# Kernel optimization log

Measured on AMD Instinct MI355X. Metric: run time of the kernel, lower is better.

## Reference

```python
import jax, jax.numpy as jnp
import numpy as np

B, T, C = 4, 2048, 1024
H = 16
D = C // H  # head_size = 64


def setup_inputs() -> dict:
    key = jax.random.key(0)
    ks = jax.random.split(key, 9)
    s = 1.0 / np.sqrt(C)  # keep activations well-scaled
    return {
        "x": jax.random.normal(ks[0], (B, T, C), dtype=jnp.float32),
        "Wq": jax.random.normal(ks[1], (C, C), dtype=jnp.float32) * s,
        "bq": jnp.zeros((C,), dtype=jnp.float32),
        "Wk": jax.random.normal(ks[2], (C, C), dtype=jnp.float32) * s,
        "bk": jnp.zeros((C,), dtype=jnp.float32),
        "Wv": jax.random.normal(ks[3], (C, C), dtype=jnp.float32) * s,
        "bv": jnp.zeros((C,), dtype=jnp.float32),
        "Wp": jax.random.normal(ks[4], (C, C), dtype=jnp.float32) * s,
        "bp": jnp.zeros((C,), dtype=jnp.float32),
    }


def reference(x, Wq, bq, Wk, bk, Wv, bv, Wp, bp):
    # QKV projections: [B,T,C] -> [B,H,T,D]
    def heads(y):
        return y.reshape(B, T, H, D).transpose(0, 2, 1, 3)

    q = heads(x @ Wq + bq)
    k = heads(x @ Wk + bk)
    v = heads(x @ Wv + bv)

    # scaled dot-product attention scores [B,H,T,T]
    attn = jnp.einsum("bhqd,bhkd->bhqk", q, k) * (D ** -0.5)
    causal = jnp.tril(jnp.ones((T, T), dtype=bool))  # [T,T]
    attn = jnp.where(causal[None, None, :, :], attn, -jnp.inf)
    attn = jax.nn.softmax(attn, axis=-1)
    # dropout = 0.0 -> identity

    y = jnp.einsum("bhqk,bhkd->bhqd", attn, v)  # [B,H,T,D]
    y = y.transpose(0, 2, 1, 3).reshape(B, T, C)
    return y @ Wp + bp
```

## Files before the change

kernel.cpp:

```cpp
#include <hip/hip_runtime.h>
#include <math.h>

static constexpr int Bsz = 4;
static constexpr int Tn  = 2048;
static constexpr int Cn  = 1024;
static constexpr int Hn  = 16;
static constexpr int Dn  = 64;

typedef __attribute__((ext_vector_type(8))) short bf16x8;
typedef __attribute__((ext_vector_type(4))) float f32x4;

#define MFMA16(a, b, c) __builtin_amdgcn_mfma_f32_16x16x32_bf16((a), (b), (c), 0, 0, 0)

static constexpr float kQScale = 0.18033688f;

__device__ __forceinline__ unsigned short f2bf(float f) {
  unsigned u = __float_as_uint(f);
  unsigned r = (u + 0x7fffu + ((u >> 16) & 1u)) >> 16;
  return (unsigned short)r;
}

__device__ __forceinline__ unsigned cvtpk_bf16(float lo, float hi) {
  unsigned r;
  asm("v_cvt_pk_bf16_f32 %0, %1, %2" : "=v"(r) : "v"(lo), "v"(hi));
  return r;
}

__device__ __forceinline__ void load_lds16(const void* g, void* l) {
  __builtin_amdgcn_global_load_lds(
      (const __attribute__((address_space(1))) void*)g,
      (__attribute__((address_space(3))) void*)l, 16, 0, 0);
}

__global__ __launch_bounds__(256) void prep_k(
    const float* __restrict__ x, unsigned short* __restrict__ xb,
    const float* __restrict__ w0, const float* __restrict__ w1,
    const float* __restrict__ w2, const float* __restrict__ w3,
    unsigned short* __restrict__ o0, unsigned short* __restrict__ o1,
    unsigned short* __restrict__ o2, unsigned short* __restrict__ o3) {
  __shared__ unsigned short Ts[64][65];
  const int z = blockIdx.z;
  if (z >= 4) {
    const int bi = (z - 4) * 256 + blockIdx.y * 16 + blockIdx.x;
    const int i = bi * 256 + threadIdx.x;
    const float4 a = ((const float4*)x)[i * 2 + 0];
    const float4 b = ((const float4*)x)[i * 2 + 1];
    uint4 o;
    o.x = cvtpk_bf16(a.x, a.y);
    o.y = cvtpk_bf16(a.z, a.w);
    o.z = cvtpk_bf16(b.x, b.y);
    o.w = cvtpk_bf16(b.z, b.w);
    ((uint4*)xb)[i] = o;
    return;
  }
  const float* W;
  unsigned short* O;
  switch (z) {
    case 0: W = w0; O = o0; break;
    case 1: W = w1; O = o1; break;
    case 2: W = w2; O = o2; break;
    default: W = w3; O = o3; break;
  }
  const int k0 = blockIdx.y * 64, n0 = blockIdx.x * 64;
  const int tid = threadIdx.x;
  const int cr = tid >> 4, cc = (tid & 15) * 4;
#pragma unroll
  for (int p = 0; p < 4; ++p) {
    const int r = p * 16 + cr;
    const float4 v = *(const float4*)&W[(size_t)(k0 + r) * Cn + n0 + cc];
    Ts[r][cc + 0] = f2bf(v.x);
    Ts[r][cc + 1] = f2bf(v.y);
    Ts[r][cc + 2] = f2bf(v.z);
    Ts[r][cc + 3] = f2bf(v.w);
  }
  __syncthreads();
#pragma unroll
  for (int p = 0; p < 4; ++p) {
    const int n = p * 16 + cr;
    ushort4 o;
    o.x = Ts[cc + 0][n];
    o.y = Ts[cc + 1][n];
    o.z = Ts[cc + 2][n];
    o.w = Ts[cc + 3][n];
    *(ushort4*)&O[(size_t)(n0 + n) * Cn + k0 + cc] = o;
  }
}

__device__ __forceinline__ void gemm_core(
    const unsigned short* __restrict__ A, const unsigned short* __restrict__ Bt,
    int row0, int col0, unsigned short* As, unsigned short* Bs,
    f32x4 acc[4][4]) {
  const int tid = threadIdx.x;
  const int lane = tid & 63, w = tid >> 6;
  const int wm = w >> 1, wn = w & 1;
  const int lr = lane & 15, lg = lane >> 4;

  auto stage = [&](int buf, int k0) {
#pragma unroll
    for (int it = 0; it < 4; ++it) {
      const int c = it * 256 + tid;
      const int r = c >> 3;
      const int lc = (c & 7) ^ (r & 7);
      load_lds16(A + (size_t)(row0 + r) * Cn + k0 + lc * 8,
                 &As[buf * 8192 + c * 8]);
    }
#pragma unroll
    for (int it = 0; it < 4; ++it) {
      const int c = it * 256 + tid;
      const int r = c >> 3;
      const int lc = (c & 7) ^ (r & 7);
      load_lds16(Bt + (size_t)(col0 + r) * Cn + k0 + lc * 8,
                 &Bs[buf * 8192 + c * 8]);
    }
  };

  stage(0, 0);
  for (int ki = 0; ki < 16; ++ki) {
    const int cur = ki & 1;
    const bool pf = (ki < 15);
    if (pf) stage(cur ^ 1, (ki + 1) * 64);
    if (pf) asm volatile("s_waitcnt vmcnt(8)" ::: "memory");
    else    asm volatile("s_waitcnt vmcnt(0)" ::: "memory");
    __builtin_amdgcn_s_barrier();
#pragma unroll
    for (int ks = 0; ks < 2; ++ks) {
      bf16x8 af[4], bfr[4];
#pragma unroll
      for (int mi = 0; mi < 4; ++mi)
        af[mi] = *(const bf16x8*)
            &As[cur * 8192 + (wm * 64 + mi * 16 + lr) * 64 +
                (((ks * 4 + lg) ^ (lr & 7)) << 3)];
#pragma unroll
      for (int ni = 0; ni < 4; ++ni)
        bfr[ni] = *(const bf16x8*)
            &Bs[cur * 8192 + (wn * 64 + ni * 16 + lr) * 64 +
                (((ks * 4 + lg) ^ (lr & 7)) << 3)];
#pragma unroll
      for (int mi = 0; mi < 4; ++mi)
#pragma unroll
        for (int ni = 0; ni < 4; ++ni)
          acc[mi][ni] = MFMA16(af[mi], bfr[ni], acc[mi][ni]);
    }
    if (pf) __builtin_amdgcn_s_barrier();
  }
}

__global__ __launch_bounds__(256, 2) void qkv_fused_k(
    const unsigned short* __restrict__ A,
    const unsigned short* __restrict__ Wq, const unsigned short* __restrict__ Wk,
    const unsigned short* __restrict__ Wv,
    const float* __restrict__ bq, const float* __restrict__ bk,
    const float* __restrict__ bv,
    unsigned short* __restrict__ Qo, unsigned short* __restrict__ Ko,
    unsigned short* __restrict__ Vo) {
  __shared__ unsigned short As[2][128 * 32];
  __shared__ unsigned short Bs[2][3][128 * 32];
  const int tid = threadIdx.x, lane = tid & 63, w = tid >> 6;
  const int wm = w >> 1, wn = w & 1;
  const int lr = lane & 15, lg = lane >> 4;
  const int row0 = blockIdx.x * 128, col0 = blockIdx.y * 128;

  auto stage = [&](int buf, int k0) {
    const unsigned short* Ws[3] = {Wq, Wk, Wv};
#pragma unroll
    for (int it = 0; it < 2; ++it) {
      const int c = it * 256 + tid;
      const int r = c >> 2;
      const int lc = (c & 3) ^ ((r >> 1) & 3);
      load_lds16(A + (size_t)(row0 + r) * Cn + k0 + lc * 8, &As[buf][c * 8]);
    }
#pragma unroll
    for (int z = 0; z < 3; ++z)
#pragma unroll
      for (int it = 0; it < 2; ++it) {
        const int c = it * 256 + tid;
        const int r = c >> 2;
        const int lc = (c & 3) ^ ((r >> 1) & 3);
        load_lds16(Ws[z] + (size_t)(col0 + r) * Cn + k0 + lc * 8,
                   &Bs[buf][z][c * 8]);
      }
  };

  const f32x4 fz = {0.f, 0.f, 0.f, 0.f};
  f32x4 acc0[4][4], acc1[4][4], acc2[4][4];
#pragma unroll
  for (int i = 0; i < 4; ++i)
#pragma unroll
    for (int j = 0; j < 4; ++j) { acc0[i][j] = fz; acc1[i][j] = fz; acc2[i][j] = fz; }

  stage(0, 0);
  for (int ki = 0; ki < 32; ++ki) {
    const int cur = ki & 1;
    const bool pf = (ki < 31);
    if (pf) stage(cur ^ 1, (ki + 1) * 32);
    if (pf) asm volatile("s_waitcnt vmcnt(8)" ::: "memory");
    else    asm volatile("s_waitcnt vmcnt(0)" ::: "memory");
    __builtin_amdgcn_s_barrier();

    const int kchunk = (lg ^ ((lr >> 1) & 3)) << 3;
    bf16x8 af[4];
#pragma unroll
    for (int mi = 0; mi < 4; ++mi)
      af[mi] = *(const bf16x8*)
          &As[cur][(wm * 64 + mi * 16 + lr) * 32 + kchunk];

    {
      bf16x8 bfr[4];
#pragma unroll
      for (int ni = 0; ni < 4; ++ni)
        bfr[ni] = *(const bf16x8*)
            &Bs[cur][0][(wn * 64 + ni * 16 + lr) * 32 + kchunk];
      __builtin_amdgcn_s_setprio(1);
#pragma unroll
      for (int mi = 0; mi < 4; ++mi)
#pragma unroll
        for (int ni = 0; ni < 4; ++ni)
          acc0[mi][ni] = MFMA16(af[mi], bfr[ni], acc0[mi][ni]);
      __builtin_amdgcn_s_setprio(0);
    }
    {
      bf16x8 bfr[4];
#pragma unroll
      for (int ni = 0; ni < 4; ++ni)
        bfr[ni] = *(const bf16x8*)
            &Bs[cur][1][(wn * 64 + ni * 16 + lr) * 32 + kchunk];
      __builtin_amdgcn_s_setprio(1);
#pragma unroll
      for (int mi = 0; mi < 4; ++mi)
#pragma unroll
        for (int ni = 0; ni < 4; ++ni)
          acc1[mi][ni] = MFMA16(af[mi], bfr[ni], acc1[mi][ni]);
      __builtin_amdgcn_s_setprio(0);
    }
    {
      bf16x8 bfr[4];
#pragma unroll
      for (int ni = 0; ni < 4; ++ni)
        bfr[ni] = *(const bf16x8*)
            &Bs[cur][2][(wn * 64 + ni * 16 + lr) * 32 + kchunk];
      __builtin_amdgcn_s_setprio(1);
#pragma unroll
      for (int mi = 0; mi < 4; ++mi)
#pragma unroll
        for (int ni = 0; ni < 4; ++ni)
          acc2[mi][ni] = MFMA16(af[mi], bfr[ni], acc2[mi][ni]);
      __builtin_amdgcn_s_setprio(0);
    }

    if (pf) __builtin_amdgcn_s_barrier();
  }

  const int b = row0 >> 11;
  const int t0w = (row0 & (Tn - 1)) + wm * 64;
  const int h = (col0 >> 6) + wn;

#pragma unroll
  for (int mi = 0; mi < 4; ++mi) {
#pragma unroll
    for (int ni = 0; ni < 4; ++ni) {
      const int d = ni * 16 + lr;
      const float bv_ = bv[col0 + wn * 64 + d];
      const int t0 = t0w + mi * 16 + lg * 4;
      ushort4 o4;
      o4.x = f2bf(acc2[mi][ni][0] + bv_);
      o4.y = f2bf(acc2[mi][ni][1] + bv_);
      o4.z = f2bf(acc2[mi][ni][2] + bv_);
      o4.w = f2bf(acc2[mi][ni][3] + bv_);
      *(ushort4*)&Vo[(((size_t)b * Hn + h) * Dn + d) * Tn + t0] = o4;
    }
  }

  __syncthreads();
  unsigned short* epi = &Bs[0][0][0] + w * 4352;

  {
#pragma unroll
    for (int mi = 0; mi < 4; ++mi)
#pragma unroll
      for (int ni = 0; ni < 4; ++ni) {
        const float bv_ = bq[col0 + wn * 64 + ni * 16 + lr];
#pragma unroll
        for (int r = 0; r < 4; ++r)
          epi[(mi * 16 + lg * 4 + r) * 68 + ni * 16 + lr] =
              f2bf((acc0[mi][ni][r] + bv_) * kQScale);
      }
    asm volatile("s_waitcnt lgkmcnt(0)" ::: "memory");
#pragma unroll
    for (int j = 0; j < 8; ++j) {
      const int t = (lane >> 3) + 8 * j;
      const int ck = lane & 7;
      const bf16x8 v = *(const bf16x8*)&epi[t * 68 + ck * 8];
      *(bf16x8*)&Qo[((((size_t)b * Hn + h) * Tn + t0w + t) << 6) + ck * 8] = v;
    }
  }
  {
#pragma unroll
    for (int mi = 0; mi < 4; ++mi)
#pragma unroll
      for (int ni = 0; ni < 4; ++ni) {
        const float bv_ = bk[col0 + wn * 64 + ni * 16 + lr];
#pragma unroll
        for (int r = 0; r < 4; ++r)
          epi[(mi * 16 + lg * 4 + r) * 68 + ni * 16 + lr] =
              f2bf(acc1[mi][ni][r] + bv_);
      }
    asm volatile("s_waitcnt lgkmcnt(0)" ::: "memory");
#pragma unroll
    for (int j = 0; j < 8; ++j) {
      const int t = (lane >> 3) + 8 * j;
      const int ck = lane & 7;
      const bf16x8 v = *(const bf16x8*)&epi[t * 68 + ck * 8];
      *(bf16x8*)&Ko[((((size_t)b * Hn + h) * Tn + t0w + t) << 6) + ck * 8] = v;
    }
  }
}

__global__ __launch_bounds__(256, 2) void proj_gemm_k(
    const unsigned short* __restrict__ A, const unsigned short* __restrict__ Bt,
    const float* __restrict__ bias, float* __restrict__ out) {
  __shared__ unsigned short As[2 * 128 * 64];
  __shared__ unsigned short Bs[2 * 128 * 64];
  const int row0 = blockIdx.x * 128, col0 = blockIdx.y * 128;
  const f32x4 fz = {0.f, 0.f, 0.f, 0.f};
  f32x4 acc[4][4];
#pragma unroll
  for (int i = 0; i < 4; ++i)
#pragma unroll
    for (int j = 0; j < 4; ++j) acc[i][j] = fz;

  gemm_core(A, Bt, row0, col0, As, Bs, acc);

  const int lane = threadIdx.x & 63, w = threadIdx.x >> 6;
  const int wm = w >> 1, wn = w & 1;
  const int lr = lane & 15, lg = lane >> 4;
#pragma unroll
  for (int mi = 0; mi < 4; ++mi) {
#pragma unroll
    for (int ni = 0; ni < 4; ++ni) {
      const int col = col0 + wn * 64 + ni * 16 + lr;
      const float bv_ = bias[col];
#pragma unroll
      for (int r = 0; r < 4; ++r) {
        const int row = row0 + wm * 64 + mi * 16 + lg * 4 + r;
        out[(size_t)row * Cn + col] = acc[mi][ni][r] + bv_;
      }
    }
  }
}

__global__ __launch_bounds__(256, 4) void attn_mfma_k(
    const unsigned short* __restrict__ Q, const unsigned short* __restrict__ K,
    const unsigned short* __restrict__ Vt, unsigned short* __restrict__ Y) {
  __shared__ unsigned short Ks[2][64 * 64];
  __shared__ unsigned short Vs[64 * 64];
  __shared__ unsigned short Ps[4][16 * 64];
  const int tid = threadIdx.x, lane = tid & 63, w = tid >> 6;
  const int lr = lane & 15, lg = lane >> 4;
  const int bh = blockIdx.x;
  const int qt = (int)gridDim.y - 1 - blockIdx.y;
  const size_t base = (size_t)bh * Tn * Dn;

  bf16x8 qf[2];
  const int qrow = qt * 64 + w * 16 + lr;
#pragma unroll
  for (int ks = 0; ks < 2; ++ks)
    qf[ks] = *(const bf16x8*)&Q[base + (size_t)qrow * Dn + ks * 32 + lg * 8];

  const short one_bf = (short)0x3F80;
  const bf16x8 onesf = {one_bf, one_bf, one_bf, one_bf,
                        one_bf, one_bf, one_bf, one_bf};

  auto stage_K = [&](int buf, int kt) {
#pragma unroll
    for (int it = 0; it < 2; ++it) {
      const int c = it * 256 + tid;
      const int r = c >> 3;
      const int lc = (c & 7) ^ (r & 7);
      load_lds16(K + base + (size_t)(kt * 64 + r) * Dn + lc * 8, &Ks[buf][c * 8]);
    }
  };
  auto stage_V = [&](int kt) {
#pragma unroll
    for (int it = 0; it < 2; ++it) {
      const int c = it * 256 + tid;
      const int r = c >> 3;
      const int lc = (c & 7) ^ (r & 7);
      load_lds16(Vt + base + (size_t)r * Tn + kt * 64 + lc * 8, &Vs[c * 8]);
    }
  };

  const f32x4 fz = {0.f, 0.f, 0.f, 0.f};
  f32x4 oacc[4];
#pragma unroll
  for (int i = 0; i < 4; ++i) oacc[i] = fz;
  f32x4 acc_l = fz;

  stage_K(0, 0);
  asm volatile("s_waitcnt vmcnt(0)" ::: "memory");
  __builtin_amdgcn_s_barrier();

  for (int kt = 0; kt <= qt; ++kt) {
    const int cur = kt & 1;
    const bool pf = (kt < qt);
    stage_V(kt);
    if (pf) stage_K(cur ^ 1, kt + 1);

    f32x4 s[4];
#pragma unroll
    for (int ni = 0; ni < 4; ++ni) s[ni] = fz;
    __builtin_amdgcn_s_setprio(1);
#pragma unroll
    for (int ni = 0; ni < 4; ++ni)
#pragma unroll
      for (int ks = 0; ks < 2; ++ks) {
        const bf16x8 kf = *(const bf16x8*)
            &Ks[cur][(ni * 16 + lr) * 64 + (((ks * 4 + lg) ^ (lr & 7)) << 3)];
        s[ni] = MFMA16(kf, qf[ks], s[ni]);
      }
    __builtin_amdgcn_s_setprio(0);

    const bool diag = (kt == qt);
    uint2 pw[4];
#pragma unroll
    for (int ni = 0; ni < 4; ++ni) {
      float p[4];
#pragma unroll
      for (int r = 0; r < 4; ++r) {
        float v = s[ni][r];
        if (diag) {
          const int gk = kt * 64 + ni * 16 + lg * 4 + r;
          if (gk > qrow) v = -1e30f;
        }
        p[r] = exp2f(v);
      }
      pw[ni].x = cvtpk_bf16(p[0], p[1]);
      pw[ni].y = cvtpk_bf16(p[2], p[3]);
    }

#pragma unroll
    for (int ni = 0; ni < 4; ++ni) {
      const int byte = lr * 128 + ((((ni * 2) + (lg >> 1)) ^ (lr & 7)) << 4) +
                       ((lg & 1) << 3);
      *(uint2*)((char*)&Ps[w][0] + byte) = pw[ni];
    }

    if (pf) asm volatile("s_waitcnt vmcnt(2)" ::: "memory");
    else    asm volatile("s_waitcnt vmcnt(0)" ::: "memory");
    __builtin_amdgcn_s_barrier();

    __builtin_amdgcn_s_setprio(1);
#pragma unroll
    for (int ks = 0; ks < 2; ++ks) {
      const bf16x8 pa = *(const bf16x8*)
          &Ps[w][lr * 64 + (((ks * 4 + lg) ^ (lr & 7)) << 3)];
      acc_l = MFMA16(pa, onesf, acc_l);
#pragma unroll
      for (int nd = 0; nd < 4; ++nd) {
        const bf16x8 vf = *(const bf16x8*)
            &Vs[(nd * 16 + lr) * 64 + (((ks * 4 + lg) ^ (lr & 7)) << 3)];
        oacc[nd] = MFMA16(pa, vf, oacc[nd]);
      }
    }
    __builtin_amdgcn_s_setprio(0);

    if (pf) {
      asm volatile("s_waitcnt vmcnt(0)" ::: "memory");
      __builtin_amdgcn_s_barrier();
    }
  }

  const int b = bh >> 4, h = bh & 15;
  unsigned short* epi = &Ks[0][0] + w * 1152;
#pragma unroll
  for (int i = 0; i < 4; ++i) {
    const float inv = 1.f / acc_l[i];
#pragma unroll
    for (int nd = 0; nd < 4; ++nd)
      epi[(lg * 4 + i) * 68 + nd * 16 + lr] = f2bf(oacc[nd][i] * inv);
  }
  asm volatile("s_waitcnt lgkmcnt(0)" ::: "memory");
#pragma unroll
  for (int j = 0; j < 2; ++j) {
    const int tl = lane >> 2;
    const int ck = (lane & 3) + 4 * j;
    const bf16x8 v = *(const bf16x8*)&epi[tl * 68 + ck * 8];
    const int t = qt * 64 + w * 16 + tl;
    *(bf16x8*)&Y[((size_t)b * Tn + t) * Cn + h * Dn + ck * 8] = v;
  }
}

extern "C" void kernel_launch(void* const* d_in, const int* in_sizes, int n_in,
                              void* d_out, int out_size, void* d_ws, size_t ws_size,
                              hipStream_t stream) {
  const float* x  = (const float*)d_in[0];
  const float* Wq = (const float*)d_in[1];
  const float* bq = (const float*)d_in[2];
  const float* Wk = (const float*)d_in[3];
  const float* bk = (const float*)d_in[4];
  const float* Wv = (const float*)d_in[5];
  const float* bv = (const float*)d_in[6];
  const float* Wp = (const float*)d_in[7];
  const float* bp = (const float*)d_in[8];
  float* out = (float*)d_out;

  const size_t xe = (size_t)Bsz * Tn * Cn;
  const size_t we = (size_t)Cn * Cn;
  unsigned short* p = (unsigned short*)d_ws;
  unsigned short* xb  = p; p += xe;
  unsigned short* Wqt = p; p += we;
  unsigned short* Wkt = p; p += we;
  unsigned short* Wvt = p; p += we;
  unsigned short* Wpt = p; p += we;
  unsigned short* Qb  = p; p += xe;
  unsigned short* Kb  = p; p += xe;
  unsigned short* Vtb = p; p += xe;
  unsigned short* Yb  = p; p += xe;

  prep_k<<<dim3(16, 16, 20), dim3(256), 0, stream>>>(
      x, xb, Wq, Wk, Wv, Wp, Wqt, Wkt, Wvt, Wpt);

  qkv_fused_k<<<dim3((Bsz * Tn) / 128, Cn / 128), dim3(256), 0, stream>>>(
      xb, Wqt, Wkt, Wvt, bq, bk, bv, Qb, Kb, Vtb);

  attn_mfma_k<<<dim3(Bsz * Hn, Tn / 64), dim3(256), 0, stream>>>(Qb, Kb, Vtb, Yb);

  proj_gemm_k<<<dim3((Bsz * Tn) / 128, Cn / 128), dim3(256), 0, stream>>>(
      Yb, Wpt, bp, out);
}
```

Measured before the change: 152.7 us.

## Stagger QKV weight-tile prefetch across the three MFMA phases

The single prefetch of the A tile plus all three weight tiles is split into staggered stages. A and Wq are issued at the start of each k-step, Wk after the Q-phase MFMAs, and Wv after the K-phase MFMAs. Each issue is gated by its own vmcnt wait and barrier, so a phase waits only for the tile it needs and load issue is spread across the compute. This adds two barriers per k-step and relies on exact vmcnt bookkeeping for correctness.

```diff
diff --git a/kernel.cpp b/kernel.cpp
--- a/kernel.cpp
+++ b/kernel.cpp
@@ -160,8 +160,7 @@
   const int lr = lane & 15, lg = lane >> 4;
   const int row0 = blockIdx.x * 128, col0 = blockIdx.y * 128;
 
-  auto stage = [&](int buf, int k0) {
-    const unsigned short* Ws[3] = {Wq, Wk, Wv};
+  auto stage_A = [&](int buf, int k0) {
 #pragma unroll
     for (int it = 0; it < 2; ++it) {
       const int c = it * 256 + tid;
@@ -169,16 +168,33 @@
       const int lc = (c & 3) ^ ((r >> 1) & 3);
       load_lds16(A + (size_t)(row0 + r) * Cn + k0 + lc * 8, &As[buf][c * 8]);
     }
-#pragma unroll
-    for (int z = 0; z < 3; ++z)
-#pragma unroll
-      for (int it = 0; it < 2; ++it) {
-        const int c = it * 256 + tid;
-        const int r = c >> 2;
-        const int lc = (c & 3) ^ ((r >> 1) & 3);
-        load_lds16(Ws[z] + (size_t)(col0 + r) * Cn + k0 + lc * 8,
-                   &Bs[buf][z][c * 8]);
-      }
+  };
+  auto stage_B0 = [&](int buf, int k0) {
+#pragma unroll
+    for (int it = 0; it < 2; ++it) {
+      const int c = it * 256 + tid;
+      const int r = c >> 2;
+      const int lc = (c & 3) ^ ((r >> 1) & 3);
+      load_lds16(Wq + (size_t)(col0 + r) * Cn + k0 + lc * 8, &Bs[buf][0][c * 8]);
+    }
+  };
+  auto stage_B1 = [&](int buf, int k0) {
+#pragma unroll
+    for (int it = 0; it < 2; ++it) {
+      const int c = it * 256 + tid;
+      const int r = c >> 2;
+      const int lc = (c & 3) ^ ((r >> 1) & 3);
+      load_lds16(Wk + (size_t)(col0 + r) * Cn + k0 + lc * 8, &Bs[buf][1][c * 8]);
+    }
+  };
+  auto stage_B2 = [&](int buf, int k0) {
+#pragma unroll
+    for (int it = 0; it < 2; ++it) {
+      const int c = it * 256 + tid;
+      const int r = c >> 2;
+      const int lc = (c & 3) ^ ((r >> 1) & 3);
+      load_lds16(Wv + (size_t)(col0 + r) * Cn + k0 + lc * 8, &Bs[buf][2][c * 8]);
+    }
   };
 
   const f32x4 fz = {0.f, 0.f, 0.f, 0.f};
@@ -188,22 +204,24 @@
 #pragma unroll
     for (int j = 0; j < 4; ++j) { acc0[i][j] = fz; acc1[i][j] = fz; acc2[i][j] = fz; }
 
-  stage(0, 0);
+  stage_A(0, 0); stage_B0(0, 0);
+  stage_B1(0, 0);
+  stage_B2(0, 0);
+
   for (int ki = 0; ki < 32; ++ki) {
     const int cur = ki & 1;
     const bool pf = (ki < 31);
-    if (pf) stage(cur ^ 1, (ki + 1) * 32);
-    if (pf) asm volatile("s_waitcnt vmcnt(8)" ::: "memory");
-    else    asm volatile("s_waitcnt vmcnt(0)" ::: "memory");
+    const int nk0 = (ki + 1) * 32;
+    const int kchunk = (lg ^ ((lr >> 1) & 3)) << 3;
+
+    asm volatile("s_waitcnt vmcnt(4)" ::: "memory");
     __builtin_amdgcn_s_barrier();
-
-    const int kchunk = (lg ^ ((lr >> 1) & 3)) << 3;
+    if (pf) { stage_A(cur ^ 1, nk0); stage_B0(cur ^ 1, nk0); }
     bf16x8 af[4];
 #pragma unroll
     for (int mi = 0; mi < 4; ++mi)
       af[mi] = *(const bf16x8*)
           &As[cur][(wm * 64 + mi * 16 + lr) * 32 + kchunk];
-
     {
       bf16x8 bfr[4];
 #pragma unroll
@@ -218,6 +236,11 @@
           acc0[mi][ni] = MFMA16(af[mi], bfr[ni], acc0[mi][ni]);
       __builtin_amdgcn_s_setprio(0);
     }
+
+    if (pf) asm volatile("s_waitcnt vmcnt(6)" ::: "memory");
+    else    asm volatile("s_waitcnt vmcnt(2)" ::: "memory");
+    __builtin_amdgcn_s_barrier();
+    if (pf) stage_B1(cur ^ 1, nk0);
     {
       bf16x8 bfr[4];
 #pragma unroll
@@ -232,6 +255,11 @@
           acc1[mi][ni] = MFMA16(af[mi], bfr[ni], acc1[mi][ni]);
       __builtin_amdgcn_s_setprio(0);
     }
+
+    if (pf) asm volatile("s_waitcnt vmcnt(6)" ::: "memory");
+    else    asm volatile("s_waitcnt vmcnt(0)" ::: "memory");
+    __builtin_amdgcn_s_barrier();
+    if (pf) stage_B2(cur ^ 1, nk0);
     {
       bf16x8 bfr[4];
 #pragma unroll
@@ -246,8 +274,6 @@
           acc2[mi][ni] = MFMA16(af[mi], bfr[ni], acc2[mi][ni]);
       __builtin_amdgcn_s_setprio(0);
     }
-
-    if (pf) __builtin_amdgcn_s_barrier();
   }
 
   const int b = row0 >> 11;
```

Result: slower. 158.1 us (+3.5%).
